# Kernel tuning notes

Measured on AMD Instinct MI355X. Metric: run time of the kernel, lower is better.

Reference implementation:

```python
import jax, jax.numpy as jnp
import numpy as np

EPS = 1e-8

def setup_inputs() -> dict:
    key = jax.random.key(0)
    k1, k2, k3 = jax.random.split(key, 3)
    central_value = jax.random.normal(k1, (256, 512), dtype=jnp.float32)
    partial_deviations = jax.random.normal(k2, (256, 256, 512), dtype=jnp.float32)
    err = jax.random.uniform(k3, (256, 512), dtype=jnp.float32)
    return {"central_value": central_value, "partial_deviations": partial_deviations, "err": err}


def reference(central_value, partial_deviations, err):
    # calculate_range: zonotope interval bounds
    radius = jnp.sum(jnp.abs(partial_deviations), axis=1) + jnp.abs(err)  # (B, D)
    lower = central_value - radius
    upper = central_value + radius

    rl = jax.nn.relu(lower)
    ru = jax.nn.relu(upper)
    lam = (ru - rl) / (upper - lower + EPS)
    lam = jnp.where(lower >= 0, 1.0, lam)
    lam = jnp.where(upper < 0, 0.0, lam)
    lam = jnp.nan_to_num(lam, nan=0.0)
    lam = jnp.clip(lam, 0.0, 1.0)
    beta = (rl - lam * lower) * 0.5
    delta = jnp.abs(beta)

    # apply_linear_approx
    new_central = lam * central_value + beta                              # (B, D)
    scaled_pd = partial_deviations * lam[:, None, :]                      # (B, N, D)
    d = central_value.shape[-1]
    diag = delta[:, :, None] * jnp.eye(d, dtype=delta.dtype)              # diag_embed -> (B, D, D)
    new_pd = jnp.concatenate([scaled_pd, diag], axis=1)                   # (B, N+D, D)
    new_err = lam * err
    return (new_central, new_pd, new_err)
```

## Files before the change

### kernel.cpp

```cpp
#include <hip/hip_runtime.h>

#define BB 256
#define NN 256
#define DD 512
#define RT (NN + DD)

constexpr float EPSF = 1e-8f;
constexpr size_t PD_OFF = (size_t)BB * DD;
constexpr size_t NE_OFF = PD_OFF + (size_t)BB * RT * DD;

typedef float vfloat4 __attribute__((ext_vector_type(4)));

__device__ __forceinline__ vfloat4 nt_load4(const vfloat4* p) {
    return __builtin_nontemporal_load(p);
}
__device__ __forceinline__ void nt_store4(vfloat4* p, vfloat4 v) {
    __builtin_nontemporal_store(v, p);
}

__global__ __launch_bounds__(256) void fused_kernel(
    const float* __restrict__ cv, const float* __restrict__ pd,
    const float* __restrict__ err, float* __restrict__ out)
{
    const int bx    = blockIdx.x;
    const int b     = bx >> 3;
    const int dbase = (bx & 7) * 64;
    const int tid   = threadIdx.x;
    const int j     = tid & 15;
    const int rb    = tid >> 4;

    const vfloat4* pdb = (const vfloat4*)(pd + (size_t)b * NN * DD + dbase);
    vfloat4 data[16];
    float ax = 0.f, ay = 0.f, az = 0.f, aw = 0.f;
#pragma unroll
    for (int k = 0; k < 16; ++k) {
        const int r = rb + (k << 4);
        vfloat4 v = nt_load4(pdb + (size_t)r * (DD / 4) + j);
        data[k] = v;
        ax += fabsf(v.x); ay += fabsf(v.y); az += fabsf(v.z); aw += fabsf(v.w);
    }
    ax += __shfl_xor(ax, 16); ay += __shfl_xor(ay, 16);
    az += __shfl_xor(az, 16); aw += __shfl_xor(aw, 16);
    ax += __shfl_xor(ax, 32); ay += __shfl_xor(ay, 32);
    az += __shfl_xor(az, 32); aw += __shfl_xor(aw, 32);

    __shared__ float part[4][64];
    __shared__ __align__(16) float lam_s[64];
    __shared__ float del_s[64];
    const int wave = tid >> 6;
    const int lane = tid & 63;
    if (lane < 16) {
        part[wave][lane * 4 + 0] = ax;
        part[wave][lane * 4 + 1] = ay;
        part[wave][lane * 4 + 2] = az;
        part[wave][lane * 4 + 3] = aw;
    }
    __syncthreads();

    if (tid < 64) {
        float rad = part[0][tid] + part[1][tid] + part[2][tid] + part[3][tid];
        const size_t gi = (size_t)b * DD + dbase + tid;
        const float c = cv[gi];
        const float e = err[gi];
        rad += fabsf(e);
        const float lo = c - rad, up = c + rad;
        const float rl = fmaxf(lo, 0.f), ru = fmaxf(up, 0.f);
        float l = (ru - rl) / (up - lo + EPSF);
        if (lo >= 0.f) l = 1.f;
        if (up <  0.f) l = 0.f;
        if (l != l)    l = 0.f;
        l = fminf(fmaxf(l, 0.f), 1.f);
        const float beta = (rl - l * lo) * 0.5f;
        out[gi]          = l * c + beta;
        out[NE_OFF + gi] = l * e;
        lam_s[tid] = l;
        del_s[tid] = fabsf(beta);
    }
    __syncthreads();

    const vfloat4 lm = *(const vfloat4*)&lam_s[j * 4];
    vfloat4* outb = (vfloat4*)(out + PD_OFF + (size_t)b * RT * DD + dbase);
#pragma unroll
    for (int k = 0; k < 16; ++k) {
        const int r = rb + (k << 4);
        vfloat4 v = data[k];
        v.x *= lm.x; v.y *= lm.y; v.z *= lm.z; v.w *= lm.w;
        nt_store4(outb + (size_t)r * (DD / 4) + j, v);
    }

    vfloat4* diagb = (vfloat4*)(out + PD_OFF + (size_t)b * RT * DD
                                + (size_t)NN * DD + dbase);
#pragma unroll
    for (int k = 0; k < 32; ++k) {
        const int i  = rb + (k << 4);
        vfloat4 v = (vfloat4)(0.f, 0.f, 0.f, 0.f);
        const int ii = i - dbase;
        if ((unsigned)ii < 64u && (ii >> 2) == j)
            v[ii & 3] = del_s[ii];
        nt_store4(diagb + (size_t)i * (DD / 4) + j, v);
    }
}

extern "C" void kernel_launch(void* const* d_in, const int* in_sizes, int n_in,
                              void* d_out, int out_size, void* d_ws, size_t ws_size,
                              hipStream_t stream) {
    const float* cv  = (const float*)d_in[0];
    const float* pd  = (const float*)d_in[1];
    const float* err = (const float*)d_in[2];
    float* out = (float*)d_out;

    fused_kernel<<<dim3(BB * 8), dim3(256), 0, stream>>>(cv, pd, err, out);
}
```

Before: 492.7 us.

## Split fused zonotope kernel into reduce, scatter and finalize kernels

New measurement: 549.7 us. 1.12x slower.

```diff
diff --git a/kernel.cpp b/kernel.cpp
--- a/kernel.cpp
+++ b/kernel.cpp
@@ -4,12 +4,14 @@
 #define NN 256
 #define DD 512
 #define RT (NN + DD)
+#define D4 (DD / 4)
 
 constexpr float EPSF = 1e-8f;
 constexpr size_t PD_OFF = (size_t)BB * DD;
 constexpr size_t NE_OFF = PD_OFF + (size_t)BB * RT * DD;
 
 typedef float vfloat4 __attribute__((ext_vector_type(4)));
+
 
 __device__ __forceinline__ vfloat4 nt_load4(const vfloat4* p) {
     return __builtin_nontemporal_load(p);
@@ -18,87 +20,115 @@
     __builtin_nontemporal_store(v, p);
 }
 
-__global__ __launch_bounds__(256) void fused_kernel(
+__device__ __forceinline__ void relax1(float rad, float c,
+                                       float& l, float& beta) {
+    const float lo = c - rad, up = c + rad;
+    const float rl = fmaxf(lo, 0.f), ru = fmaxf(up, 0.f);
+    l = (ru - rl) / (up - lo + EPSF);
+    if (lo >= 0.f) l = 1.f;
+    if (up <  0.f) l = 0.f;
+    if (l != l)    l = 0.f;
+    l = fminf(fmaxf(l, 0.f), 1.f);
+    beta = (rl - l * lo) * 0.5f;
+}
+
+__global__ __launch_bounds__(1024) void reduce_kernel(
     const float* __restrict__ cv, const float* __restrict__ pd,
     const float* __restrict__ err, float* __restrict__ out)
 {
-    const int bx    = blockIdx.x;
-    const int b     = bx >> 3;
-    const int dbase = (bx & 7) * 64;
-    const int tid   = threadIdx.x;
-    const int j     = tid & 15;
-    const int rb    = tid >> 4;
+    const int b   = blockIdx.x;
+    const int tid = threadIdx.x;
+    const int d4  = tid & (D4 - 1);
+    const int rg  = tid >> 7;
 
-    const vfloat4* pdb = (const vfloat4*)(pd + (size_t)b * NN * DD + dbase);
-    vfloat4 data[16];
+    const vfloat4* pdb = (const vfloat4*)pd + (size_t)b * NN * D4;
     float ax = 0.f, ay = 0.f, az = 0.f, aw = 0.f;
-#pragma unroll
-    for (int k = 0; k < 16; ++k) {
-        const int r = rb + (k << 4);
-        vfloat4 v = nt_load4(pdb + (size_t)r * (DD / 4) + j);
-        data[k] = v;
+#pragma unroll 8
+    for (int it = 0; it < NN / 8; ++it) {
+        vfloat4 v = nt_load4(pdb + (size_t)((it << 3) + rg) * D4 + d4);
         ax += fabsf(v.x); ay += fabsf(v.y); az += fabsf(v.z); aw += fabsf(v.w);
     }
-    ax += __shfl_xor(ax, 16); ay += __shfl_xor(ay, 16);
-    az += __shfl_xor(az, 16); aw += __shfl_xor(aw, 16);
-    ax += __shfl_xor(ax, 32); ay += __shfl_xor(ay, 32);
-    az += __shfl_xor(az, 32); aw += __shfl_xor(aw, 32);
 
-    __shared__ float part[4][64];
-    __shared__ __align__(16) float lam_s[64];
-    __shared__ float del_s[64];
-    const int wave = tid >> 6;
-    const int lane = tid & 63;
-    if (lane < 16) {
-        part[wave][lane * 4 + 0] = ax;
-        part[wave][lane * 4 + 1] = ay;
-        part[wave][lane * 4 + 2] = az;
-        part[wave][lane * 4 + 3] = aw;
+    __shared__ vfloat4 part[8][D4];
+    {
+        vfloat4 s;
+        s.x = ax; s.y = ay; s.z = az; s.w = aw;
+        part[rg][d4] = s;
     }
     __syncthreads();
 
-    if (tid < 64) {
-        float rad = part[0][tid] + part[1][tid] + part[2][tid] + part[3][tid];
-        const size_t gi = (size_t)b * DD + dbase + tid;
-        const float c = cv[gi];
-        const float e = err[gi];
-        rad += fabsf(e);
-        const float lo = c - rad, up = c + rad;
-        const float rl = fmaxf(lo, 0.f), ru = fmaxf(up, 0.f);
-        float l = (ru - rl) / (up - lo + EPSF);
-        if (lo >= 0.f) l = 1.f;
-        if (up <  0.f) l = 0.f;
-        if (l != l)    l = 0.f;
-        l = fminf(fmaxf(l, 0.f), 1.f);
-        const float beta = (rl - l * lo) * 0.5f;
-        out[gi]          = l * c + beta;
-        out[NE_OFF + gi] = l * e;
-        lam_s[tid] = l;
-        del_s[tid] = fabsf(beta);
+    if (tid < D4) {
+        vfloat4 rad = part[0][tid];
+#pragma unroll
+        for (int g = 1; g < 8; ++g) {
+            vfloat4 p = part[g][tid];
+            rad.x += p.x; rad.y += p.y; rad.z += p.z; rad.w += p.w;
+        }
+        const size_t gi4 = (size_t)b * D4 + tid;
+        const vfloat4 c = ((const vfloat4*)cv)[gi4];
+        const vfloat4 e = ((const vfloat4*)err)[gi4];
+        vfloat4 l4, b4;
+        float l, beta;
+        relax1(rad.x + fabsf(e.x), c.x, l, beta);  l4.x = l; b4.x = beta;
+        relax1(rad.y + fabsf(e.y), c.y, l, beta);  l4.y = l; b4.y = beta;
+        relax1(rad.z + fabsf(e.z), c.z, l, beta);  l4.z = l; b4.z = beta;
+        relax1(rad.w + fabsf(e.w), c.w, l, beta);  l4.w = l; b4.w = beta;
+        ((vfloat4*)(out + NE_OFF))[gi4] = l4;
+        ((vfloat4*)out)[gi4]            = b4;
     }
-    __syncthreads();
+}
 
-    const vfloat4 lm = *(const vfloat4*)&lam_s[j * 4];
-    vfloat4* outb = (vfloat4*)(out + PD_OFF + (size_t)b * RT * DD + dbase);
-#pragma unroll
-    for (int k = 0; k < 16; ++k) {
-        const int r = rb + (k << 4);
-        vfloat4 v = data[k];
-        v.x *= lm.x; v.y *= lm.y; v.z *= lm.z; v.w *= lm.w;
-        nt_store4(outb + (size_t)r * (DD / 4) + j, v);
+#define WBLOCKS 2048
+#define RPB (BB * RT / WBLOCKS)
+
+__global__ __launch_bounds__(256) void pd_kernel(
+    const float* __restrict__ pd, float* out )
+{
+    const int bx  = blockIdx.x;
+    const int b   = bx >> 3;
+    const int tid = threadIdx.x;
+    const int d4  = tid & (D4 - 1);
+    const int ro  = tid >> 7;
+
+    const vfloat4 lm  = ((const vfloat4*)(out + NE_OFF))[(size_t)b * D4 + d4];
+    const float*  bet = out + (size_t)b * DD;
+    const vfloat4* pdb  = (const vfloat4*)pd + (size_t)b * NN * D4;
+    vfloat4*       outb = (vfloat4*)(out + PD_OFF) + (size_t)b * RT * D4;
+
+    int r = (bx & 7) * RPB + ro;
+#pragma unroll 4
+    for (int i = 0; i < RPB / 2; ++i, r += 2) {
+        vfloat4 v;
+        if (r < NN) {
+            vfloat4 pv = nt_load4(pdb + (size_t)r * D4 + d4);
+            v.x = pv.x * lm.x; v.y = pv.y * lm.y;
+            v.z = pv.z * lm.z; v.w = pv.w * lm.w;
+        } else {
+            const int dg = r - NN;
+            v.x = 0.f; v.y = 0.f; v.z = 0.f; v.w = 0.f;
+            if (d4 == (dg >> 2))
+                v[dg & 3] = fabsf(bet[dg]);
+        }
+        nt_store4(outb + (size_t)r * D4 + d4, v);
     }
+}
 
-    vfloat4* diagb = (vfloat4*)(out + PD_OFF + (size_t)b * RT * DD
-                                + (size_t)NN * DD + dbase);
-#pragma unroll
-    for (int k = 0; k < 32; ++k) {
-        const int i  = rb + (k << 4);
-        vfloat4 v = (vfloat4)(0.f, 0.f, 0.f, 0.f);
-        const int ii = i - dbase;
-        if ((unsigned)ii < 64u && (ii >> 2) == j)
-            v[ii & 3] = del_s[ii];
-        nt_store4(diagb + (size_t)i * (DD / 4) + j, v);
-    }
+__global__ __launch_bounds__(256) void finalize_kernel(
+    const float* __restrict__ cv, const float* __restrict__ err,
+    float* out )
+{
+    const size_t i = (size_t)blockIdx.x * 256 + threadIdx.x;
+    const vfloat4 l  = ((const vfloat4*)(out + NE_OFF))[i];
+    const vfloat4 bt = ((const vfloat4*)out)[i];
+    const vfloat4 c  = ((const vfloat4*)cv)[i];
+    const vfloat4 e  = ((const vfloat4*)err)[i];
+    vfloat4 nc, ne;
+    nc.x = l.x * c.x + bt.x;  ne.x = l.x * e.x;
+    nc.y = l.y * c.y + bt.y;  ne.y = l.y * e.y;
+    nc.z = l.z * c.z + bt.z;  ne.z = l.z * e.z;
+    nc.w = l.w * c.w + bt.w;  ne.w = l.w * e.w;
+    ((vfloat4*)out)[i]            = nc;
+    ((vfloat4*)(out + NE_OFF))[i] = ne;
 }
 
 extern "C" void kernel_launch(void* const* d_in, const int* in_sizes, int n_in,
@@ -109,5 +139,7 @@
     const float* err = (const float*)d_in[2];
     float* out = (float*)d_out;
 
-    fused_kernel<<<dim3(BB * 8), dim3(256), 0, stream>>>(cv, pd, err, out);
+    reduce_kernel<<<dim3(BB), dim3(1024), 0, stream>>>(cv, pd, err, out);
+    pd_kernel<<<dim3(WBLOCKS), dim3(256), 0, stream>>>(pd, out);
+    finalize_kernel<<<dim3(BB * DD / 4 / 256), dim3(256), 0, stream>>>(cv, err, out);
 }
```
